# Performance work log

Measured on AMD Instinct MI355X. Metric: run time of the kernel, lower is better.

Reference implementation:

```python
import jax, jax.numpy as jnp
import numpy as np

N_NODES = 100000
N_EDGES = 1600000
IN_DIM = 128
HID = 128
N_CLASSES = 40


def setup_inputs() -> dict:
    key = jax.random.key(0)
    ks = jax.random.split(key, 8)
    s = 1.0 / np.sqrt(IN_DIM)
    return {
        "x": jax.random.normal(ks[0], (N_NODES, IN_DIM), jnp.float32),
        "edge_index": jax.random.randint(ks[1], (2, N_EDGES), 0, N_NODES, dtype=jnp.int32),
        "W1": jax.random.normal(ks[2], (IN_DIM, HID), jnp.float32) * s,
        "b1": jnp.zeros((HID,), jnp.float32),
        "W2": jax.random.normal(ks[3], (HID, HID), jnp.float32) * s,
        "b2": jnp.zeros((HID,), jnp.float32),
        "Wout": jax.random.normal(ks[4], (HID, N_CLASSES), jnp.float32) * s,
        "bout": jnp.zeros((N_CLASSES,), jnp.float32),
    }


def gcn_norm(edge_index, num_nodes):
    # PyG gcn_norm: add self loops (weight 1), symmetric deg^-1/2 normalization.
    loops = jnp.arange(num_nodes, dtype=edge_index.dtype)
    row = jnp.concatenate([edge_index[0], loops])  # source j
    col = jnp.concatenate([edge_index[1], loops])  # target i
    ones = jnp.ones(row.shape[0], jnp.float32)
    deg = jax.ops.segment_sum(ones, col, num_segments=num_nodes)
    dinv = jnp.where(deg > 0, jax.lax.rsqrt(jnp.maximum(deg, 1.0)), 0.0)
    norm = dinv[row] * dinv[col]
    return row, col, norm


def gcn_layer(x, row, col, norm, W, b):
    h = x @ W                                  # [N, HID] linear (bias=False)
    msg = norm[:, None] * h[row]               # gather x_j + edge-weight scale
    agg = jax.ops.segment_sum(msg, col, num_segments=x.shape[0])  # scatter-add
    return agg + b


def reference(x, edge_index, W1, b1, W2, b2, Wout, bout):
    n = x.shape[0]
    row, col, norm = gcn_norm(edge_index, n)
    x = jax.nn.relu(gcn_layer(x, row, col, norm, W1, b1))
    x = jax.nn.relu(gcn_layer(x, row, col, norm, W2, b2))
    return x @ Wout + bout
```

## Files before the change

### kernel.cpp

```cpp
#include <hip/hip_runtime.h>
#include <hip/hip_bf16.h>
#include <hip/hip_fp16.h>

#define NBKT 512

typedef _Float16 f16x8 __attribute__((ext_vector_type(8)));
typedef float f32x4 __attribute__((ext_vector_type(4)));


__global__ __launch_bounds__(256) void k_bktA1(const int* __restrict__ ecol,
                                               int* __restrict__ blkBkt, int E, int chunk,
                                               const float* __restrict__ W1,
                                               const float* __restrict__ W2,
                                               const float* __restrict__ Wout,
                                               __half* __restrict__ Wt1,
                                               __half* __restrict__ Wt2,
                                               __half* __restrict__ WtO) {
  int t = threadIdx.x;
  if (blockIdx.x < 256) {
    __shared__ int h[NBKT];
    h[t] = 0;
    h[t + 256] = 0;
    __syncthreads();
    int s = blockIdx.x * chunk, e = min(s + chunk, E);
    for (int i = s + t; i < e; i += 256) atomicAdd(&h[ecol[i] >> 8], 1);
    __syncthreads();
    blkBkt[blockIdx.x * NBKT + t] = h[t];
    blkBkt[blockIdx.x * NBKT + t + 256] = h[t + 256];
  } else {
    int id = (blockIdx.x - 256) * 256 + t;
    if (id < 32768) {
      const float* W = (id < 16384) ? W1 : W2;
      __half* Wt = (id < 16384) ? Wt1 : Wt2;
      int i = id & 16383;
      int k = i >> 7, c = i & 127;
      Wt[c * 128 + k] = __float2half(W[i]);
    } else if (id < 38912) {
      int i = id - 32768;
      int c = i >> 7, k = i & 127;
      WtO[i] = (c < 40) ? __float2half(Wout[k * 40 + c]) : __half(0.0f);
    }
  }
}

__global__ __launch_bounds__(256) void k_bktA2a(int* __restrict__ blkBkt,
                                                int* __restrict__ bktTotal) {
  __shared__ int buf[2][256];
  int b = blockIdx.x, t = threadIdx.x;
  int x = blkBkt[t * NBKT + b];
  int cur = 0;
  buf[0][t] = x;
  __syncthreads();
  int v = x;
  for (int off = 1; off < 256; off <<= 1) {
    v = buf[cur][t];
    if (t >= off) v += buf[cur][t - off];
    buf[cur ^ 1][t] = v;
    cur ^= 1;
    __syncthreads();
  }
  blkBkt[t * NBKT + b] = v - x;
  if (t == 255) bktTotal[b] = v;
}

__global__ __launch_bounds__(512) void k_bktA2b(const int* __restrict__ bktTotal,
                                                int* __restrict__ bktBase,
                                                int* __restrict__ offs, int N, int E) {
  __shared__ int buf[2][512];
  int t = threadIdx.x;
  int x = bktTotal[t];
  int cur = 0;
  buf[0][t] = x;
  __syncthreads();
  int v = x;
  for (int off = 1; off < 512; off <<= 1) {
    v = buf[cur][t];
    if (t >= off) v += buf[cur][t - off];
    buf[cur ^ 1][t] = v;
    cur ^= 1;
    __syncthreads();
  }
  bktBase[t] = v - x;
  if (t == 511) bktBase[512] = v;
  if (t == 0) offs[N] = E;
}

__global__ __launch_bounds__(256) void k_bktA3(const int* __restrict__ erow,
                                               const int* __restrict__ ecol,
                                               const int* __restrict__ blkBkt,
                                               const int* __restrict__ bktBase,
                                               uint* __restrict__ ebuf, int E, int chunk) {
  __shared__ int cur[NBKT];
  int t = threadIdx.x;
  cur[t] = bktBase[t] + blkBkt[blockIdx.x * NBKT + t];
  cur[t + 256] = bktBase[t + 256] + blkBkt[blockIdx.x * NBKT + t + 256];
  __syncthreads();
  int s = blockIdx.x * chunk, e = min(s + chunk, E);
  for (int i = s + t; i < e; i += 256) {
    int c = ecol[i], r = erow[i];
    int pos = atomicAdd(&cur[c >> 8], 1);
    ebuf[pos] = ((uint)(c & 255) << 17) | (uint)r;
  }
}

__global__ __launch_bounds__(256) void k_bktB1(const uint* __restrict__ ebuf,
                                               const int* __restrict__ bktBase,
                                               float* __restrict__ dinv,
                                               int* __restrict__ offs, int N) {
  __shared__ int cnt[256];
  __shared__ int buf[2][256];
  int b = blockIdx.x, t = threadIdx.x;
  int node0 = b << 8;
  cnt[t] = 0;
  __syncthreads();
  int s = bktBase[b], e = bktBase[b + 1];
  for (int i = s + t; i < e; i += 256) atomicAdd(&cnt[ebuf[i] >> 17], 1);
  __syncthreads();
  int x = cnt[t];
  if (node0 + t < N) dinv[node0 + t] = rsqrtf((float)x + 1.0f);
  int cur = 0;
  buf[0][t] = x;
  __syncthreads();
  int v = x;
  for (int off = 1; off < 256; off <<= 1) {
    v = buf[cur][t];
    if (t >= off) v += buf[cur][t - off];
    buf[cur ^ 1][t] = v;
    cur ^= 1;
    __syncthreads();
  }
  if (node0 + t < N) offs[node0 + t] = s + v - x;
}

__global__ __launch_bounds__(256) void k_bktB2(const uint* __restrict__ ebuf,
                                               const int* __restrict__ bktBase,
                                               const int* __restrict__ offs,
                                               const float* __restrict__ dinv,
                                               uint* __restrict__ adj, int N) {
  __shared__ int cur[256];
  int b = blockIdx.x, t = threadIdx.x;
  int node0 = b << 8;
  cur[t] = (node0 + t < N) ? offs[node0 + t] : 0;
  __syncthreads();
  int s = bktBase[b], e = bktBase[b + 1];
  for (int i = s + t; i < e; i += 256) {
    uint ent = ebuf[i];
    int clow = (int)(ent >> 17);
    int r = (int)(ent & 0x1FFFFu);
    int pos = atomicAdd(&cur[clow], 1);
    float w = dinv[r] * dinv[node0 + clow];
    uint q = (uint)fminf(w * 65536.0f + 0.5f, 32767.0f);
    adj[pos] = (q << 17) | (uint)r;
  }
}


template <int A_F32>
__global__ __launch_bounds__(256) void k_gemm_mfma(const void* __restrict__ Aptr,
                                                   const __half* __restrict__ Wt,
                                                   __half* __restrict__ C, int n) {
  __shared__ __half Cs[4][16][136];
  int t = threadIdx.x;
  int wv = t >> 6, l = t & 63;
  int lr = l & 15, lg = l >> 4;

  f16x8 B[8][4];
#pragma unroll
  for (int nt = 0; nt < 8; ++nt)
#pragma unroll
    for (int ks = 0; ks < 4; ++ks)
      B[nt][ks] = *reinterpret_cast<const f16x8*>(Wt + (nt * 16 + lr) * 128 + ks * 32 + lg * 8);

  int ntiles = (n + 15) >> 4;
  int wgid = blockIdx.x * 4 + wv;
  int wstride = gridDim.x * 4;

  float4 rf_c[8], rf_n[8];
  f16x8 rh_c[4], rh_n[4];

  auto loadA = [&](int tile, float4* rf, f16x8* rh) {
    int arow = tile * 16 + lr;
    int crow = arow < n ? arow : 0;
    if (A_F32) {
      const float* A = (const float*)Aptr + (size_t)crow * 128 + lg * 8;
#pragma unroll
      for (int ks = 0; ks < 4; ++ks) {
        rf[ks * 2] = *reinterpret_cast<const float4*>(A + ks * 32);
        rf[ks * 2 + 1] = *reinterpret_cast<const float4*>(A + ks * 32 + 4);
      }
    } else {
      const __half* A = (const __half*)Aptr + (size_t)crow * 128 + lg * 8;
#pragma unroll
      for (int ks = 0; ks < 4; ++ks) rh[ks] = *reinterpret_cast<const f16x8*>(A + ks * 32);
    }
  };

  if (wgid < ntiles) loadA(wgid, rf_c, rh_c);

  for (int tile = wgid; tile < ntiles; tile += wstride) {
    int tnext = tile + wstride;
    if (tnext < ntiles) loadA(tnext, rf_n, rh_n);

    f16x8 a[4];
    if (A_F32) {
#pragma unroll
      for (int ks = 0; ks < 4; ++ks) {
        float4 u0 = rf_c[ks * 2], u1 = rf_c[ks * 2 + 1];
        f16x8 av;
        av[0] = (_Float16)u0.x; av[1] = (_Float16)u0.y;
        av[2] = (_Float16)u0.z; av[3] = (_Float16)u0.w;
        av[4] = (_Float16)u1.x; av[5] = (_Float16)u1.y;
        av[6] = (_Float16)u1.z; av[7] = (_Float16)u1.w;
        a[ks] = av;
      }
    } else {
#pragma unroll
      for (int ks = 0; ks < 4; ++ks) a[ks] = rh_c[ks];
    }

    f32x4 acc[8];
#pragma unroll
    for (int nt = 0; nt < 8; ++nt) acc[nt] = (f32x4){0.f, 0.f, 0.f, 0.f};
#pragma unroll
    for (int ks = 0; ks < 4; ++ks)
#pragma unroll
      for (int nt = 0; nt < 8; ++nt)
        acc[nt] = __builtin_amdgcn_mfma_f32_16x16x32_f16(a[ks], B[nt][ks], acc[nt], 0, 0, 0);

#pragma unroll
    for (int nt = 0; nt < 8; ++nt)
#pragma unroll
      for (int r = 0; r < 4; ++r)
        Cs[wv][lg * 4 + r][nt * 16 + lr] = __float2half(acc[nt][r]);
#pragma unroll
    for (int j = 0; j < 4; ++j) {
      int row = j * 4 + lg;
      int gr = tile * 16 + row;
      if (gr < n)
        *reinterpret_cast<uint4*>(&C[(size_t)gr * 128 + lr * 8]) =
            *reinterpret_cast<const uint4*>(&Cs[wv][row][lr * 8]);
    }

    if (A_F32) {
#pragma unroll
      for (int j = 0; j < 8; ++j) rf_c[j] = rf_n[j];
    } else {
#pragma unroll
      for (int j = 0; j < 4; ++j) rh_c[j] = rh_n[j];
    }
  }
}


__global__ __launch_bounds__(256) void k_agg(const __half* __restrict__ h,
                                             const int* __restrict__ offs,
                                             const uint* __restrict__ adj,
                                             const float* __restrict__ dinv,
                                             const float* __restrict__ bias,
                                             __half* __restrict__ out, int n) {
  int wid = (blockIdx.x * blockDim.x + threadIdx.x) >> 6;
  wid = __builtin_amdgcn_readfirstlane(wid);
  int lane = threadIdx.x & 63;
  if (wid >= n) return;
  const __half2* hv = reinterpret_cast<const __half2*>(h);
  float ddst = dinv[wid];
  float w0 = ddst * ddst;
  float2 acc = __half22float2(hv[(size_t)wid * 64 + lane]);
  acc.x *= w0;
  acc.y *= w0;
  int s = offs[wid], e = offs[wid + 1];
  int cnt = e - s;
  const uint* ap = adj + s;
  const float qs = 1.0f / 65536.0f;

  float wm[8];
  __half2 hg[8];
#pragma unroll
  for (int j = 0; j < 8; ++j) {
    uint a = ap[j];
    bool v = j < cnt;
    int src = v ? (int)(a & 0x1FFFFu) : wid;
    wm[j] = v ? (float)(a >> 17) * qs : 0.f;
    hg[j] = hv[(size_t)src * 64 + lane];
  }
  for (int k0 = 0; k0 < cnt; k0 += 8) {
    int k1 = k0 + 8;
    bool more = k1 < cnt;
    float wn[8];
    __half2 hn[8];
    if (more) {
#pragma unroll
      for (int j = 0; j < 8; ++j) {
        uint a = ap[k1 + j];
        bool v = k1 + j < cnt;
        int src = v ? (int)(a & 0x1FFFFu) : wid;
        wn[j] = v ? (float)(a >> 17) * qs : 0.f;
        hn[j] = hv[(size_t)src * 64 + lane];
      }
    }
#pragma unroll
    for (int j = 0; j < 8; ++j) {
      float2 f = __half22float2(hg[j]);
      acc.x = fmaf(wm[j], f.x, acc.x);
      acc.y = fmaf(wm[j], f.y, acc.y);
    }
    if (more) {
#pragma unroll
      for (int j = 0; j < 8; ++j) {
        wm[j] = wn[j];
        hg[j] = hn[j];
      }
    }
  }

  float2 b = reinterpret_cast<const float2*>(bias)[lane];
  acc.x = fmaxf(acc.x + b.x, 0.f);
  acc.y = fmaxf(acc.y + b.y, 0.f);
  reinterpret_cast<__half2*>(out + (size_t)wid * 128)[lane] = __floats2half2_rn(acc.x, acc.y);
}


__global__ __launch_bounds__(256) void k_gemm_out(const __half* __restrict__ Z,
                                                  const __half* __restrict__ WtO,
                                                  const float* __restrict__ bout,
                                                  float* __restrict__ out, int n) {
  __shared__ float Cs[4][16][52];
  int t = threadIdx.x;
  int wv = t >> 6, l = t & 63;
  int lr = l & 15, lg = l >> 4;

  f16x8 B[3][4];
#pragma unroll
  for (int nt = 0; nt < 3; ++nt)
#pragma unroll
    for (int ks = 0; ks < 4; ++ks)
      B[nt][ks] = *reinterpret_cast<const f16x8*>(WtO + (nt * 16 + lr) * 128 + ks * 32 + lg * 8);

  float bb[3];
#pragma unroll
  for (int nt = 0; nt < 3; ++nt) {
    int c = nt * 16 + lr;
    bb[nt] = (c < 40) ? bout[c] : 0.f;
  }

  int ntiles = (n + 15) >> 4;
  int wgid = blockIdx.x * 4 + wv;
  int wstride = gridDim.x * 4;

  f16x8 rh_c[4], rh_n[4];
  auto loadA = [&](int tile, f16x8* rh) {
    int arow = tile * 16 + lr;
    int crow = arow < n ? arow : 0;
    const __half* A = Z + (size_t)crow * 128 + lg * 8;
#pragma unroll
    for (int ks = 0; ks < 4; ++ks) rh[ks] = *reinterpret_cast<const f16x8*>(A + ks * 32);
  };

  if (wgid < ntiles) loadA(wgid, rh_c);

  for (int tile = wgid; tile < ntiles; tile += wstride) {
    int tnext = tile + wstride;
    if (tnext < ntiles) loadA(tnext, rh_n);

    f32x4 acc[3];
#pragma unroll
    for (int nt = 0; nt < 3; ++nt) acc[nt] = (f32x4){0.f, 0.f, 0.f, 0.f};
#pragma unroll
    for (int ks = 0; ks < 4; ++ks)
#pragma unroll
      for (int nt = 0; nt < 3; ++nt)
        acc[nt] = __builtin_amdgcn_mfma_f32_16x16x32_f16(rh_c[ks], B[nt][ks], acc[nt], 0, 0, 0);

#pragma unroll
    for (int nt = 0; nt < 3; ++nt)
#pragma unroll
      for (int r = 0; r < 4; ++r)
        Cs[wv][lg * 4 + r][nt * 16 + lr] = acc[nt][r] + bb[nt];
#pragma unroll
    for (int j = 0; j < 3; ++j) {
      int f = l + j * 64;
      if (f < 160) {
        int row = f / 10, c4 = f - row * 10;
        int gr = tile * 16 + row;
        if (gr < n)
          *reinterpret_cast<float4*>(&out[(size_t)gr * 40 + c4 * 4]) =
              *reinterpret_cast<const float4*>(&Cs[wv][row][c4 * 4]);
      }
    }
#pragma unroll
    for (int j = 0; j < 4; ++j) rh_c[j] = rh_n[j];
  }
}


extern "C" void kernel_launch(void* const* d_in, const int* in_sizes, int n_in,
                              void* d_out, int out_size, void* d_ws, size_t ws_size,
                              hipStream_t stream) {
  const float* x = (const float*)d_in[0];
  const int* ei = (const int*)d_in[1];
  const float* W1 = (const float*)d_in[2];
  const float* b1 = (const float*)d_in[3];
  const float* W2 = (const float*)d_in[4];
  const float* b2 = (const float*)d_in[5];
  const float* Wout = (const float*)d_in[6];
  const float* bout = (const float*)d_in[7];
  float* out = (float*)d_out;

  const int N = in_sizes[0] / 128;
  const int E = in_sizes[1] / 2;
  const int* erow = ei;
  const int* ecol = ei + E;

  char* ws = (char*)d_ws;
  size_t off = 0;
  auto alloc = [&](size_t bytes) -> void* {
    void* p = ws + off;
    off = (off + bytes + 255) & ~(size_t)255;
    return p;
  };
  int* blkBkt = (int*)alloc((size_t)256 * NBKT * 4);
  int* bktTotal = (int*)alloc(NBKT * 4);
  int* bktBase = (int*)alloc((NBKT + 1) * 4);
  int* offs = (int*)alloc((size_t)(N + 1) * 4);
  float* dinv = (float*)alloc((size_t)N * 4);
  uint* ebuf = (uint*)alloc((size_t)E * 4);
  uint* adj = (uint*)alloc((size_t)(E + 8) * 4);
  __half* Wt1 = (__half*)alloc(128 * 128 * 2);
  __half* Wt2 = (__half*)alloc(128 * 128 * 2);
  __half* WtO = (__half*)alloc(48 * 128 * 2);
  __half* bufH = (__half*)alloc((size_t)N * 128 * 2);
  __half* bufZ = (__half*)alloc((size_t)N * 128 * 2);

  int chunk = (E + 255) / 256;
  int nbk = (N + 255) >> 8;

  k_bktA1<<<256 + 152, 256, 0, stream>>>(ecol, blkBkt, E, chunk, W1, W2, Wout,
                                         Wt1, Wt2, WtO);
  k_bktA2a<<<NBKT, 256, 0, stream>>>(blkBkt, bktTotal);
  k_bktA2b<<<1, 512, 0, stream>>>(bktTotal, bktBase, offs, N, E);
  k_bktA3<<<256, 256, 0, stream>>>(erow, ecol, blkBkt, bktBase, ebuf, E, chunk);
  k_bktB1<<<nbk, 256, 0, stream>>>(ebuf, bktBase, dinv, offs, N);
  k_bktB2<<<nbk, 256, 0, stream>>>(ebuf, bktBase, offs, dinv, adj, N);

  k_gemm_mfma<1><<<512, 256, 0, stream>>>(x, Wt1, bufH, N);
  k_agg<<<(N + 3) / 4, 256, 0, stream>>>(bufH, offs, adj, dinv, b1, bufZ, N);
  k_gemm_mfma<0><<<512, 256, 0, stream>>>(bufZ, Wt2, bufH, N);
  k_agg<<<(N + 3) / 4, 256, 0, stream>>>(bufH, offs, adj, dinv, b2, bufZ, N);
  k_gemm_out<<<512, 256, 0, stream>>>(bufZ, WtO, bout, out, N);
}
```

Measured before the change: 217.8 us.

## Fuse output projection GEMM into second aggregation kernel

The second aggregation kernel now, when templated with FUSE_OUT, writes each node's aggregated row to shared memory and multiplies it by the output weights with MFMA instructions inside the same wave. The separate k_gemm_out launch and the half-precision Z round trip through global memory are removed. In exchange, each wave loads the full output weight fragment into registers and runs a 16-row MFMA in which only one row is useful, so most of the matrix work is wasted. The higher register pressure may also reduce occupancy of the bandwidth-bound gather.

```diff
diff --git a/kernel.cpp b/kernel.cpp
--- a/kernel.cpp
+++ b/kernel.cpp
@@ -252,16 +252,37 @@
 }
 
 
+template <int FUSE_OUT>
 __global__ __launch_bounds__(256) void k_agg(const __half* __restrict__ h,
                                              const int* __restrict__ offs,
                                              const uint* __restrict__ adj,
                                              const float* __restrict__ dinv,
                                              const float* __restrict__ bias,
-                                             __half* __restrict__ out, int n) {
-  int wid = (blockIdx.x * blockDim.x + threadIdx.x) >> 6;
+                                             __half* __restrict__ outz,
+                                             const __half* __restrict__ WtO,
+                                             const float* __restrict__ bout,
+                                             float* __restrict__ outf, int n) {
+  int t = threadIdx.x;
+  int wid = (blockIdx.x * blockDim.x + t) >> 6;
   wid = __builtin_amdgcn_readfirstlane(wid);
-  int lane = threadIdx.x & 63;
+  int lane = t & 63;
   if (wid >= n) return;
+
+  f16x8 Bf[3][4];
+  float bb[3];
+  if (FUSE_OUT) {
+    int lr = lane & 15, lg = lane >> 4;
+#pragma unroll
+    for (int nt = 0; nt < 3; ++nt) {
+#pragma unroll
+      for (int ks = 0; ks < 4; ++ks)
+        Bf[nt][ks] =
+            *reinterpret_cast<const f16x8*>(WtO + (nt * 16 + lr) * 128 + ks * 32 + lg * 8);
+      int c = nt * 16 + lr;
+      bb[nt] = (c < 40) ? bout[c] : 0.f;
+    }
+  }
+
   const __half2* hv = reinterpret_cast<const __half2*>(h);
   float ddst = dinv[wid];
   float w0 = ddst * ddst;
@@ -316,79 +337,34 @@
   float2 b = reinterpret_cast<const float2*>(bias)[lane];
   acc.x = fmaxf(acc.x + b.x, 0.f);
   acc.y = fmaxf(acc.y + b.y, 0.f);
-  reinterpret_cast<__half2*>(out + (size_t)wid * 128)[lane] = __floats2half2_rn(acc.x, acc.y);
-}
-
-
-__global__ __launch_bounds__(256) void k_gemm_out(const __half* __restrict__ Z,
-                                                  const __half* __restrict__ WtO,
-                                                  const float* __restrict__ bout,
-                                                  float* __restrict__ out, int n) {
-  __shared__ float Cs[4][16][52];
-  int t = threadIdx.x;
-  int wv = t >> 6, l = t & 63;
-  int lr = l & 15, lg = l >> 4;
-
-  f16x8 B[3][4];
-#pragma unroll
-  for (int nt = 0; nt < 3; ++nt)
+
+  if (!FUSE_OUT) {
+    reinterpret_cast<__half2*>(outz + (size_t)wid * 128)[lane] =
+        __floats2half2_rn(acc.x, acc.y);
+  } else {
+    __shared__ __half zs[4][136];
+    int wv = t >> 6;
+    *reinterpret_cast<__half2*>(&zs[wv][2 * lane]) = __floats2half2_rn(acc.x, acc.y);
+    int lg = lane >> 4;
+    f16x8 a[4];
 #pragma unroll
     for (int ks = 0; ks < 4; ++ks)
-      B[nt][ks] = *reinterpret_cast<const f16x8*>(WtO + (nt * 16 + lr) * 128 + ks * 32 + lg * 8);
-
-  float bb[3];
-#pragma unroll
-  for (int nt = 0; nt < 3; ++nt) {
-    int c = nt * 16 + lr;
-    bb[nt] = (c < 40) ? bout[c] : 0.f;
-  }
-
-  int ntiles = (n + 15) >> 4;
-  int wgid = blockIdx.x * 4 + wv;
-  int wstride = gridDim.x * 4;
-
-  f16x8 rh_c[4], rh_n[4];
-  auto loadA = [&](int tile, f16x8* rh) {
-    int arow = tile * 16 + lr;
-    int crow = arow < n ? arow : 0;
-    const __half* A = Z + (size_t)crow * 128 + lg * 8;
-#pragma unroll
-    for (int ks = 0; ks < 4; ++ks) rh[ks] = *reinterpret_cast<const f16x8*>(A + ks * 32);
-  };
-
-  if (wgid < ntiles) loadA(wgid, rh_c);
-
-  for (int tile = wgid; tile < ntiles; tile += wstride) {
-    int tnext = tile + wstride;
-    if (tnext < ntiles) loadA(tnext, rh_n);
-
-    f32x4 acc[3];
-#pragma unroll
-    for (int nt = 0; nt < 3; ++nt) acc[nt] = (f32x4){0.f, 0.f, 0.f, 0.f};
+      a[ks] = *reinterpret_cast<const f16x8*>(&zs[wv][ks * 32 + lg * 8]);
+    f32x4 acc3[3];
+#pragma unroll
+    for (int nt = 0; nt < 3; ++nt) acc3[nt] = (f32x4){0.f, 0.f, 0.f, 0.f};
 #pragma unroll
     for (int ks = 0; ks < 4; ++ks)
 #pragma unroll
       for (int nt = 0; nt < 3; ++nt)
-        acc[nt] = __builtin_amdgcn_mfma_f32_16x16x32_f16(rh_c[ks], B[nt][ks], acc[nt], 0, 0, 0);
-
-#pragma unroll
-    for (int nt = 0; nt < 3; ++nt)
-#pragma unroll
-      for (int r = 0; r < 4; ++r)
-        Cs[wv][lg * 4 + r][nt * 16 + lr] = acc[nt][r] + bb[nt];
-#pragma unroll
-    for (int j = 0; j < 3; ++j) {
-      int f = l + j * 64;
-      if (f < 160) {
-        int row = f / 10, c4 = f - row * 10;
-        int gr = tile * 16 + row;
-        if (gr < n)
-          *reinterpret_cast<float4*>(&out[(size_t)gr * 40 + c4 * 4]) =
-              *reinterpret_cast<const float4*>(&Cs[wv][row][c4 * 4]);
+        acc3[nt] = __builtin_amdgcn_mfma_f32_16x16x32_f16(a[ks], Bf[nt][ks], acc3[nt], 0, 0, 0);
+    if (lane < 16) {
+#pragma unroll
+      for (int nt = 0; nt < 3; ++nt) {
+        int c = nt * 16 + lane;
+        if (c < 40) outf[(size_t)wid * 40 + c] = acc3[nt][0] + bb[nt];
       }
     }
-#pragma unroll
-    for (int j = 0; j < 4; ++j) rh_c[j] = rh_n[j];
   }
 }
 
@@ -443,8 +419,9 @@
   k_bktB2<<<nbk, 256, 0, stream>>>(ebuf, bktBase, offs, dinv, adj, N);
 
   k_gemm_mfma<1><<<512, 256, 0, stream>>>(x, Wt1, bufH, N);
-  k_agg<<<(N + 3) / 4, 256, 0, stream>>>(bufH, offs, adj, dinv, b1, bufZ, N);
+  k_agg<0><<<(N + 3) / 4, 256, 0, stream>>>(bufH, offs, adj, dinv, b1, bufZ,
+                                            nullptr, nullptr, nullptr, N);
   k_gemm_mfma<0><<<512, 256, 0, stream>>>(bufZ, Wt2, bufH, N);
-  k_agg<<<(N + 3) / 4, 256, 0, stream>>>(bufH, offs, adj, dinv, b2, bufZ, N);
-  k_gemm_out<<<512, 256, 0, stream>>>(bufZ, WtO, bout, out, N);
-}
+  k_agg<1><<<(N + 3) / 4, 256, 0, stream>>>(bufH, offs, adj, dinv, b2, nullptr,
+                                            WtO, bout, out, N);
+}
```

Result: slower. 320.8 us (+47.3%).

## Fuse first GEMM into histogram kernel and merge bucket scans via last-block

Applied to the files above, without the earlier changes.

Moves the first-layer GEMM (x@W1, reading W1 directly and converting to fp16 in registers) into the same launch as the edge bucket histogram and weight transposes. The two scan kernels become one: the last block to finish, detected with an atomic counter, does the 512-bucket total scan. This removes two launches and lets the independent GEMM overlap with the histogram work. The cost is a strided gather of W1 per block and a heavier fused kernel whose shared memory use may lower occupancy.

```diff
diff --git a/kernel.cpp b/kernel.cpp
--- a/kernel.cpp
+++ b/kernel.cpp
@@ -8,44 +8,126 @@
 typedef float f32x4 __attribute__((ext_vector_type(4)));
 
 
-__global__ __launch_bounds__(256) void k_bktA1(const int* __restrict__ ecol,
-                                               int* __restrict__ blkBkt, int E, int chunk,
-                                               const float* __restrict__ W1,
-                                               const float* __restrict__ W2,
-                                               const float* __restrict__ Wout,
-                                               __half* __restrict__ Wt1,
-                                               __half* __restrict__ Wt2,
-                                               __half* __restrict__ WtO) {
+__global__ __launch_bounds__(256) void k_fused1(const float* __restrict__ X,
+                                                const float* __restrict__ W1,
+                                                const int* __restrict__ ecol,
+                                                int* __restrict__ blkBkt, int E, int chunk,
+                                                const float* __restrict__ W2,
+                                                const float* __restrict__ Wout,
+                                                __half* __restrict__ Wt2,
+                                                __half* __restrict__ WtO,
+                                                __half* __restrict__ C, int n,
+                                                int* __restrict__ done) {
+  __shared__ __half Cs[4][16][136];
+  __shared__ int h[NBKT];
   int t = threadIdx.x;
-  if (blockIdx.x < 256) {
-    __shared__ int h[NBKT];
+  int bid = blockIdx.x;
+
+  if (bid < 512) {
+    int wv = t >> 6, l = t & 63;
+    int lr = l & 15, lg = l >> 4;
+    f16x8 B[8][4];
+#pragma unroll
+    for (int nt = 0; nt < 8; ++nt)
+#pragma unroll
+      for (int ks = 0; ks < 4; ++ks) {
+        f16x8 av;
+#pragma unroll
+        for (int j = 0; j < 8; ++j)
+          av[j] = (_Float16)W1[(ks * 32 + lg * 8 + j) * 128 + nt * 16 + lr];
+        B[nt][ks] = av;
+      }
+
+    int ntiles = (n + 15) >> 4;
+    int wgid = bid * 4 + wv;
+    const int wstride = 512 * 4;
+
+    float4 rf_c[8], rf_n[8];
+    auto loadA = [&](int tile, float4* rf) {
+      int arow = tile * 16 + lr;
+      int crow = arow < n ? arow : 0;
+      const float* A = X + (size_t)crow * 128 + lg * 8;
+#pragma unroll
+      for (int ks = 0; ks < 4; ++ks) {
+        rf[ks * 2] = *reinterpret_cast<const float4*>(A + ks * 32);
+        rf[ks * 2 + 1] = *reinterpret_cast<const float4*>(A + ks * 32 + 4);
+      }
+    };
+
+    if (wgid < ntiles) loadA(wgid, rf_c);
+
+    for (int tile = wgid; tile < ntiles; tile += wstride) {
+      int tnext = tile + wstride;
+      if (tnext < ntiles) loadA(tnext, rf_n);
+
+      f16x8 a[4];
+#pragma unroll
+      for (int ks = 0; ks < 4; ++ks) {
+        float4 u0 = rf_c[ks * 2], u1 = rf_c[ks * 2 + 1];
+        f16x8 av;
+        av[0] = (_Float16)u0.x; av[1] = (_Float16)u0.y;
+        av[2] = (_Float16)u0.z; av[3] = (_Float16)u0.w;
+        av[4] = (_Float16)u1.x; av[5] = (_Float16)u1.y;
+        av[6] = (_Float16)u1.z; av[7] = (_Float16)u1.w;
+        a[ks] = av;
+      }
+
+      f32x4 acc[8];
+#pragma unroll
+      for (int nt = 0; nt < 8; ++nt) acc[nt] = (f32x4){0.f, 0.f, 0.f, 0.f};
+#pragma unroll
+      for (int ks = 0; ks < 4; ++ks)
+#pragma unroll
+        for (int nt = 0; nt < 8; ++nt)
+          acc[nt] = __builtin_amdgcn_mfma_f32_16x16x32_f16(a[ks], B[nt][ks], acc[nt], 0, 0, 0);
+
+#pragma unroll
+      for (int nt = 0; nt < 8; ++nt)
+#pragma unroll
+        for (int r = 0; r < 4; ++r)
+          Cs[wv][lg * 4 + r][nt * 16 + lr] = __float2half(acc[nt][r]);
+#pragma unroll
+      for (int j = 0; j < 4; ++j) {
+        int row = j * 4 + lg;
+        int gr = tile * 16 + row;
+        if (gr < n)
+          *reinterpret_cast<uint4*>(&C[(size_t)gr * 128 + lr * 8]) =
+              *reinterpret_cast<const uint4*>(&Cs[wv][row][lr * 8]);
+      }
+#pragma unroll
+      for (int j = 0; j < 8; ++j) rf_c[j] = rf_n[j];
+    }
+  } else if (bid < 768) {
+    int hb = bid - 512;
     h[t] = 0;
     h[t + 256] = 0;
     __syncthreads();
-    int s = blockIdx.x * chunk, e = min(s + chunk, E);
+    int s = hb * chunk, e = min(s + chunk, E);
     for (int i = s + t; i < e; i += 256) atomicAdd(&h[ecol[i] >> 8], 1);
     __syncthreads();
-    blkBkt[blockIdx.x * NBKT + t] = h[t];
-    blkBkt[blockIdx.x * NBKT + t + 256] = h[t + 256];
+    blkBkt[hb * NBKT + t] = h[t];
+    blkBkt[hb * NBKT + t + 256] = h[t + 256];
   } else {
-    int id = (blockIdx.x - 256) * 256 + t;
-    if (id < 32768) {
-      const float* W = (id < 16384) ? W1 : W2;
-      __half* Wt = (id < 16384) ? Wt1 : Wt2;
-      int i = id & 16383;
-      int k = i >> 7, c = i & 127;
-      Wt[c * 128 + k] = __float2half(W[i]);
-    } else if (id < 38912) {
-      int i = id - 32768;
+    if (bid == 768 && t == 0) *done = 0;
+    int id = (bid - 768) * 256 + t;
+    if (id < 16384) {
+      int k = id >> 7, c = id & 127;
+      Wt2[c * 128 + k] = __float2half(W2[id]);
+    } else if (id < 22528) {
+      int i = id - 16384;
       int c = i >> 7, k = i & 127;
       WtO[i] = (c < 40) ? __float2half(Wout[k * 40 + c]) : __half(0.0f);
     }
   }
 }
 
-__global__ __launch_bounds__(256) void k_bktA2a(int* __restrict__ blkBkt,
-                                                int* __restrict__ bktTotal) {
+__global__ __launch_bounds__(256) void k_A2ab(int* __restrict__ blkBkt,
+                                              int* __restrict__ bktTotal,
+                                              int* __restrict__ bktBase,
+                                              int* __restrict__ offs,
+                                              int* __restrict__ done, int N, int E) {
   __shared__ int buf[2][256];
+  __shared__ int lastFlag;
   int b = blockIdx.x, t = threadIdx.x;
   int x = blkBkt[t * NBKT + b];
   int cur = 0;
@@ -60,29 +142,43 @@
     __syncthreads();
   }
   blkBkt[t * NBKT + b] = v - x;
-  if (t == 255) bktTotal[b] = v;
-}
-
-__global__ __launch_bounds__(512) void k_bktA2b(const int* __restrict__ bktTotal,
-                                                int* __restrict__ bktBase,
-                                                int* __restrict__ offs, int N, int E) {
-  __shared__ int buf[2][512];
-  int t = threadIdx.x;
-  int x = bktTotal[t];
-  int cur = 0;
-  buf[0][t] = x;
-  __syncthreads();
-  int v = x;
-  for (int off = 1; off < 512; off <<= 1) {
-    v = buf[cur][t];
-    if (t >= off) v += buf[cur][t - off];
-    buf[cur ^ 1][t] = v;
-    cur ^= 1;
-    __syncthreads();
-  }
-  bktBase[t] = v - x;
-  if (t == 511) bktBase[512] = v;
-  if (t == 0) offs[N] = E;
+  if (t == 255) atomicExch(&bktTotal[b], v);
+  __syncthreads();
+  if (t == 0) lastFlag = (atomicAdd(done, 1) == NBKT - 1);
+  __syncthreads();
+  if (lastFlag) {
+    int x0 = atomicAdd(&bktTotal[t], 0);
+    int x1 = atomicAdd(&bktTotal[t + 256], 0);
+    int c2 = 0;
+    buf[0][t] = x0;
+    __syncthreads();
+    int v0 = x0;
+    for (int off = 1; off < 256; off <<= 1) {
+      v0 = buf[c2][t];
+      if (t >= off) v0 += buf[c2][t - off];
+      buf[c2 ^ 1][t] = v0;
+      c2 ^= 1;
+      __syncthreads();
+    }
+    bktBase[t] = v0 - x0;
+    __shared__ int sumA;
+    if (t == 255) sumA = v0;
+    __syncthreads();
+    int c3 = 0;
+    buf[0][t] = x1;
+    __syncthreads();
+    int v1 = x1;
+    for (int off = 1; off < 256; off <<= 1) {
+      v1 = buf[c3][t];
+      if (t >= off) v1 += buf[c3][t - off];
+      buf[c3 ^ 1][t] = v1;
+      c3 ^= 1;
+      __syncthreads();
+    }
+    bktBase[256 + t] = sumA + v1 - x1;
+    if (t == 255) bktBase[512] = sumA + v1;
+    if (t == 0) offs[N] = E;
+  }
 }
 
 __global__ __launch_bounds__(256) void k_bktA3(const int* __restrict__ erow,
@@ -154,9 +250,7 @@
   }
 }
 
-
-template <int A_F32>
-__global__ __launch_bounds__(256) void k_gemm_mfma(const void* __restrict__ Aptr,
+__global__ __launch_bounds__(256) void k_gemm_mfma(const __half* __restrict__ Aptr,
                                                    const __half* __restrict__ Wt,
                                                    __half* __restrict__ C, int n) {
   __shared__ __half Cs[4][16][136];
@@ -175,48 +269,20 @@
   int wgid = blockIdx.x * 4 + wv;
   int wstride = gridDim.x * 4;
 
-  float4 rf_c[8], rf_n[8];
   f16x8 rh_c[4], rh_n[4];
-
-  auto loadA = [&](int tile, float4* rf, f16x8* rh) {
+  auto loadA = [&](int tile, f16x8* rh) {
     int arow = tile * 16 + lr;
     int crow = arow < n ? arow : 0;
-    if (A_F32) {
-      const float* A = (const float*)Aptr + (size_t)crow * 128 + lg * 8;
-#pragma unroll
-      for (int ks = 0; ks < 4; ++ks) {
-        rf[ks * 2] = *reinterpret_cast<const float4*>(A + ks * 32);
-        rf[ks * 2 + 1] = *reinterpret_cast<const float4*>(A + ks * 32 + 4);
-      }
-    } else {
-      const __half* A = (const __half*)Aptr + (size_t)crow * 128 + lg * 8;
-#pragma unroll
-      for (int ks = 0; ks < 4; ++ks) rh[ks] = *reinterpret_cast<const f16x8*>(A + ks * 32);
-    }
+    const __half* A = Aptr + (size_t)crow * 128 + lg * 8;
+#pragma unroll
+    for (int ks = 0; ks < 4; ++ks) rh[ks] = *reinterpret_cast<const f16x8*>(A + ks * 32);
   };
 
-  if (wgid < ntiles) loadA(wgid, rf_c, rh_c);
+  if (wgid < ntiles) loadA(wgid, rh_c);
 
   for (int tile = wgid; tile < ntiles; tile += wstride) {
     int tnext = tile + wstride;
-    if (tnext < ntiles) loadA(tnext, rf_n, rh_n);
-
-    f16x8 a[4];
-    if (A_F32) {
-#pragma unroll
-      for (int ks = 0; ks < 4; ++ks) {
-        float4 u0 = rf_c[ks * 2], u1 = rf_c[ks * 2 + 1];
-        f16x8 av;
-        av[0] = (_Float16)u0.x; av[1] = (_Float16)u0.y;
-        av[2] = (_Float16)u0.z; av[3] = (_Float16)u0.w;
-        av[4] = (_Float16)u1.x; av[5] = (_Float16)u1.y;
-        av[6] = (_Float16)u1.z; av[7] = (_Float16)u1.w;
-        a[ks] = av;
-      }
-    } else {
-#pragma unroll
-      for (int ks = 0; ks < 4; ++ks) a[ks] = rh_c[ks];
-    }
+    if (tnext < ntiles) loadA(tnext, rh_n);
 
     f32x4 acc[8];
 #pragma unroll
@@ -225,7 +291,7 @@
     for (int ks = 0; ks < 4; ++ks)
 #pragma unroll
       for (int nt = 0; nt < 8; ++nt)
-        acc[nt] = __builtin_amdgcn_mfma_f32_16x16x32_f16(a[ks], B[nt][ks], acc[nt], 0, 0, 0);
+        acc[nt] = __builtin_amdgcn_mfma_f32_16x16x32_f16(rh_c[ks], B[nt][ks], acc[nt], 0, 0, 0);
 
 #pragma unroll
     for (int nt = 0; nt < 8; ++nt)
@@ -240,14 +306,8 @@
         *reinterpret_cast<uint4*>(&C[(size_t)gr * 128 + lr * 8]) =
             *reinterpret_cast<const uint4*>(&Cs[wv][row][lr * 8]);
     }
-
-    if (A_F32) {
-#pragma unroll
-      for (int j = 0; j < 8; ++j) rf_c[j] = rf_n[j];
-    } else {
-#pragma unroll
-      for (int j = 0; j < 4; ++j) rh_c[j] = rh_n[j];
-    }
+#pragma unroll
+    for (int j = 0; j < 4; ++j) rh_c[j] = rh_n[j];
   }
 }
 
@@ -319,7 +379,6 @@
   reinterpret_cast<__half2*>(out + (size_t)wid * 128)[lane] = __floats2half2_rn(acc.x, acc.y);
 }
 
-
 __global__ __launch_bounds__(256) void k_gemm_out(const __half* __restrict__ Z,
                                                   const __half* __restrict__ WtO,
                                                   const float* __restrict__ bout,
@@ -425,26 +484,23 @@
   float* dinv = (float*)alloc((size_t)N * 4);
   uint* ebuf = (uint*)alloc((size_t)E * 4);
   uint* adj = (uint*)alloc((size_t)(E + 8) * 4);
-  __half* Wt1 = (__half*)alloc(128 * 128 * 2);
   __half* Wt2 = (__half*)alloc(128 * 128 * 2);
   __half* WtO = (__half*)alloc(48 * 128 * 2);
   __half* bufH = (__half*)alloc((size_t)N * 128 * 2);
   __half* bufZ = (__half*)alloc((size_t)N * 128 * 2);
+  int* scanDone = (int*)alloc(4);
 
   int chunk = (E + 255) / 256;
   int nbk = (N + 255) >> 8;
 
-  k_bktA1<<<256 + 152, 256, 0, stream>>>(ecol, blkBkt, E, chunk, W1, W2, Wout,
-                                         Wt1, Wt2, WtO);
-  k_bktA2a<<<NBKT, 256, 0, stream>>>(blkBkt, bktTotal);
-  k_bktA2b<<<1, 512, 0, stream>>>(bktTotal, bktBase, offs, N, E);
+  k_fused1<<<856, 256, 0, stream>>>(x, W1, ecol, blkBkt, E, chunk, W2, Wout,
+                                    Wt2, WtO, bufH, N, scanDone);
+  k_A2ab<<<NBKT, 256, 0, stream>>>(blkBkt, bktTotal, bktBase, offs, scanDone, N, E);
   k_bktA3<<<256, 256, 0, stream>>>(erow, ecol, blkBkt, bktBase, ebuf, E, chunk);
   k_bktB1<<<nbk, 256, 0, stream>>>(ebuf, bktBase, dinv, offs, N);
   k_bktB2<<<nbk, 256, 0, stream>>>(ebuf, bktBase, offs, dinv, adj, N);
-
-  k_gemm_mfma<1><<<512, 256, 0, stream>>>(x, Wt1, bufH, N);
   k_agg<<<(N + 3) / 4, 256, 0, stream>>>(bufH, offs, adj, dinv, b1, bufZ, N);
-  k_gemm_mfma<0><<<512, 256, 0, stream>>>(bufZ, Wt2, bufH, N);
+  k_gemm_mfma<<<512, 256, 0, stream>>>(bufZ, Wt2, bufH, N);
   k_agg<<<(N + 3) / 4, 256, 0, stream>>>(bufH, offs, adj, dinv, b2, bufZ, N);
   k_gemm_out<<<512, 256, 0, stream>>>(bufZ, WtO, bout, out, N);
 }
```

After: 219.4 us. Within noise of the previous version (+0.8%).
